# Performance work log

Hardware: AMD Instinct MI355X
Metric: run time of the kernel (lower is better)

The kernel has to match this reference:

```python
import jax, jax.numpy as jnp
import numpy as np

K = 4            # number of candidate kernels in Dynamic_conv2d
TEMP = 34.0      # softmax temperature (default in Dynamic_conv2d)
C = 64           # channel


def _dyn_conv(x, w, fc1_w, fc2_w, fc2_b, pad, dil):
    """Dynamic_conv2d forward.
    x: [B,Cin,H,W]; w: [K,Cout,Cin,k,k]; fc1_w: [hid,Cin]; fc2_w: [K,hid]; fc2_b: [K].
    """
    pooled = x.mean(axis=(2, 3))                                   # [B,Cin] adaptive avg pool
    h = jax.nn.relu(jnp.einsum('bc,hc->bh', pooled, fc1_w))        # [B,hid]
    logits = jnp.einsum('bh,kh->bk', h, fc2_w) + fc2_b             # [B,K]
    att = jax.nn.softmax(logits / TEMP, axis=-1)                   # [B,K]
    agg_w = jnp.einsum('bk,koihw->boihw', att, w)                  # per-sample kernel [B,Cout,Cin,k,k]

    def conv_one(xi, wi):
        return jax.lax.conv_general_dilated(
            xi[None], wi, window_strides=(1, 1),
            padding=[(pad, pad), (pad, pad)], rhs_dilation=(dil, dil),
            dimension_numbers=('NCHW', 'OIHW', 'NCHW'))[0]

    return jax.vmap(conv_one)(x, agg_w)                            # [B,Cout,H,W]


def _leaky(v):
    return jnp.where(v >= 0, v, 0.1 * v)


def _mk_params(key, cin, cout):
    hid = int(cin * 0.25) + 1
    k1, k2, k3, k4 = jax.random.split(key, 4)
    scale = np.sqrt(2.0 / (cin * 9)).astype(np.float32)
    w = jax.random.normal(k1, (K, cout, cin, 3, 3), jnp.float32) * scale
    fc1 = jax.random.normal(k2, (hid, cin), jnp.float32) * np.sqrt(2.0 / cin).astype(np.float32)
    fc2w = jax.random.normal(k3, (K, hid), jnp.float32) * np.sqrt(2.0 / hid).astype(np.float32)
    fc2b = jnp.zeros((K,), jnp.float32)
    return w, fc1, fc2w, fc2b


def setup_inputs() -> dict:
    key = jax.random.key(0)
    ks = jax.random.split(key, 5)
    x = jax.random.normal(ks[0], (16, C, 128, 128), jnp.float32)
    out = {'x': x}
    for i, (kk, cin) in enumerate(zip(ks[1:4], [C, C, C]), start=1):
        w, fc1, fc2w, fc2b = _mk_params(kk, cin, C)
        out[f'w{i}'], out[f'fc1_{i}'], out[f'fc2w_{i}'], out[f'fc2b_{i}'] = w, fc1, fc2w, fc2b
    w, fc1, fc2w, fc2b = _mk_params(ks[4], 3 * C, C)
    out['wt'], out['fc1_t'], out['fc2w_t'], out['fc2b_t'] = w, fc1, fc2w, fc2b
    return out


def reference(x, w1, fc1_1, fc2w_1, fc2b_1, w2, fc1_2, fc2w_2, fc2b_2,
              w3, fc1_3, fc2w_3, fc2b_3, wt, fc1_t, fc2w_t, fc2b_t):
    b1 = _leaky(_dyn_conv(x, w1, fc1_1, fc2w_1, fc2b_1, pad=1, dil=1))
    b2 = _leaky(_dyn_conv(x, w2, fc1_2, fc2w_2, fc2b_2, pad=2, dil=2))
    b3 = _leaky(_dyn_conv(x, w3, fc1_3, fc2w_3, fc2b_3, pad=4, dil=4))
    cat = jnp.concatenate([b1, b2, b3], axis=1)                    # [B,3C,H,W]
    return x + _dyn_conv(cat, wt, fc1_t, fc2w_t, fc2b_t, pad=1, dil=1)
```

## Files before the change

### kernel.cpp

```cpp
#include <hip/hip_runtime.h>
#include <hip/hip_bf16.h>

typedef __hip_bfloat16 bf16;
typedef __attribute__((ext_vector_type(4))) float f32x4;
typedef __attribute__((ext_vector_type(8))) short bf16x8;
typedef __attribute__((ext_vector_type(4))) short s16x4;

#define BB 16
#define HH 128
#define WW 128
#define HWSZ (HH*WW)
#define XH 136
#define XW 136
#define XPAD 4
#define CHH 130
#define CWD 130
#define CPAD 1
#define CATC 192

__device__ __forceinline__ void zero_border_body(bf16* __restrict__ base, int HP, int WP,
                                                 int PAD, int Cdim, int slots)
{
    int cg8 = Cdim >> 3;
    int per_b = slots * cg8;
    int idx = blockIdx.x * 256 + threadIdx.x;
    if (idx >= BB * per_b) return;
    int b = idx / per_b;
    int rem = idx - b * per_b;
    int slot = rem / cg8;
    int cg = rem - slot * cg8;
    int top = PAD * WP;
    int h, w;
    if (slot < top)            { h = slot / WP;            w = slot % WP; }
    else if (slot < 2 * top)   { int s = slot - top;       h = HP - PAD + s / WP; w = s % WP; }
    else {
        int s = slot - 2 * top;
        int row = s / (2 * PAD), t = s - row * (2 * PAD);
        h = PAD + row;
        w = (t < PAD) ? t : (WP - 2 * PAD + t);
    }
    bf16x8 z = {0,0,0,0,0,0,0,0};
    *(bf16x8*)(base + (((size_t)b * HP + h) * WP + w) * Cdim + cg * 8) = z;
}

__global__ void init_borders(bf16* __restrict__ xT, bf16* __restrict__ catT,
                             float* __restrict__ pooledx, float* __restrict__ pooledc)
{
    if (blockIdx.y == 0) {
        if (blockIdx.x == 0) {
            for (int i = threadIdx.x; i < BB * 64;   i += 256) pooledx[i] = 0.f;
            for (int i = threadIdx.x; i < BB * CATC; i += 256) pooledc[i] = 0.f;
        }
        zero_border_body(xT,   XH,  XW,  XPAD, 64,   2112);
    } else {
        zero_border_body(catT, CHH, CWD, CPAD, CATC, 516);
    }
}

__global__ __launch_bounds__(256)
void transpose_pad_pool_x(const float* __restrict__ x, bf16* __restrict__ xT,
                          float* __restrict__ pooledx)
{
    __shared__ float tile[128 * 65];
    const int h = blockIdx.x, b = blockIdx.y;
    const int t = threadIdx.x;
    const int w  = t & 127;
    const int chalf = t >> 7;

    const float* xb = x + (((size_t)b * 64) * HH + h) * WW + w;
    #pragma unroll
    for (int it = 0; it < 32; ++it) {
        int c = it * 2 + chalf;
        tile[w * 65 + c] = xb[(size_t)c * HWSZ];
    }
    __syncthreads();

    bf16* dst = xT + (((size_t)b * XH + (h + XPAD)) * XW + XPAD) * 64;
    #pragma unroll
    for (int it = 0; it < 4; ++it) {
        int v  = t + it * 256;
        int ww = v >> 3;
        int c0 = (v & 7) * 8;
        const float* src = tile + ww * 65 + c0;
        bf16x8 pk;
        #pragma unroll
        for (int j = 0; j < 8; ++j)
            pk[j] = __builtin_bit_cast(short, __float2bfloat16(src[j]));
        *(bf16x8*)(dst + (size_t)ww * 64 + c0) = pk;
    }

    if (t < 64) {
        float s = 0.f;
        #pragma unroll 4
        for (int ww = 0; ww < 128; ++ww) s += tile[ww * 65 + t];
        atomicAdd(pooledx + b * 64 + t, s);
    }
}

__device__ __forceinline__ void attn_body(int b, const float* pooled, int Cin,
                                          const float* fc1, int hid,
                                          const float* fc2w, const float* fc2b,
                                          float* att, float* sp, float* sh, float* slg)
{
    for (int c = threadIdx.x; c < Cin; c += 64) sp[c] = pooled[b * Cin + c];
    __syncthreads();
    int j = threadIdx.x;
    if (j < hid) {
        float s = 0.f;
        const float4* f4 = (const float4*)(fc1 + (size_t)j * Cin);
        for (int c4 = 0; c4 < Cin / 4; ++c4) {
            float4 v = f4[c4];
            s += v.x * sp[c4*4+0] + v.y * sp[c4*4+1] + v.z * sp[c4*4+2] + v.w * sp[c4*4+3];
        }
        sh[j] = s > 0.f ? s * (1.0f / 16384.0f) : 0.f;
    }
    __syncthreads();
    int k = threadIdx.x;
    if (k < 4) {
        float s = fc2b[k];
        for (int jj = 0; jj < hid; ++jj) s += fc2w[k * hid + jj] * sh[jj];
        slg[k] = s * (1.0f / 34.0f);
    }
    __syncthreads();
    if (threadIdx.x == 0) {
        float m = fmaxf(fmaxf(slg[0], slg[1]), fmaxf(slg[2], slg[3]));
        float e0 = expf(slg[0]-m), e1 = expf(slg[1]-m), e2 = expf(slg[2]-m), e3 = expf(slg[3]-m);
        float inv = 1.0f / (e0+e1+e2+e3);
        att[b*4+0] = e0*inv; att[b*4+1] = e1*inv; att[b*4+2] = e2*inv; att[b*4+3] = e3*inv;
    }
}

__global__ void attention3(const float* __restrict__ pooled,
                           const float* f1a, const float* f2a, const float* ba, float* aa,
                           const float* f1b, const float* f2b, const float* bb, float* ab,
                           const float* f1c, const float* f2c, const float* bc, float* ac)
{
    __shared__ float sp[192], sh[64], slg[4];
    int br = blockIdx.y;
    const float* fc1  = br == 0 ? f1a : br == 1 ? f1b : f1c;
    const float* fc2w = br == 0 ? f2a : br == 1 ? f2b : f2c;
    const float* fc2b = br == 0 ? ba  : br == 1 ? bb  : bc;
    float* att        = br == 0 ? aa  : br == 1 ? ab  : ac;
    attn_body(blockIdx.x, pooled, 64, fc1, 17, fc2w, fc2b, att, sp, sh, slg);
}

__global__ void attention_one(const float* __restrict__ pooled, int Cin,
                              const float* __restrict__ fc1, int hid,
                              const float* __restrict__ fc2w,
                              const float* __restrict__ fc2b, float* __restrict__ att)
{
    __shared__ float sp[192], sh[64], slg[4];
    attn_body(blockIdx.x, pooled, Cin, fc1, hid, fc2w, fc2b, att, sp, sh, slg);
}

template<int CIN, bool PERM>
__device__ __forceinline__ void aggw_body(const float* __restrict__ w,
                                          const float* __restrict__ att,
                                          bf16* __restrict__ out, float* wl)
{
    constexpr int C9 = CIN * 9;
    constexpr int NS = (CIN / 32) * 9;
    const int co = blockIdx.x, b = blockIdx.y;
    const int src = PERM ? ((co & 15) * 4 + (co >> 4)) : co;
    for (int i = threadIdx.x; i < 4 * C9; i += 256) {
        int k = i / C9, rem = i - k * C9;
        wl[i] = w[((size_t)k * 64 + src) * C9 + rem];
    }
    __syncthreads();
    float a0 = att[b*4+0], a1 = att[b*4+1], a2 = att[b*4+2], a3 = att[b*4+3];
    const int m = co >> 4, l15 = co & 15;
    char* ob = (char*)out + (size_t)b * NS * 4096;
    for (int t = threadIdx.x; t < NS * 32; t += 256) {
        int s = t >> 5, rem = t & 31;
        int gg = rem >> 3, j = rem & 7;
        int chunk = s / 9, tap = s - chunk * 9;
        int ci = chunk * 32 + gg * 8 + j;
        float v = a0 * wl[ci*9 + tap] + a1 * wl[C9 + ci*9 + tap]
                + a2 * wl[2*C9 + ci*9 + tap] + a3 * wl[3*C9 + ci*9 + tap];
        *(bf16*)(ob + ((size_t)((s*4 + m) * 64 + (gg*16 + l15))) * 16 + j * 2) = __float2bfloat16(v);
    }
}

__global__ void aggw_frag3(const float* __restrict__ w1, const float* __restrict__ att1, bf16* o1,
                           const float* __restrict__ w2, const float* __restrict__ att2, bf16* o2,
                           const float* __restrict__ w3, const float* __restrict__ att3, bf16* o3)
{
    __shared__ float wl[4 * 64 * 9];
    int z = blockIdx.z;
    if (z == 0)      aggw_body<64, true>(w1, att1, o1, wl);
    else if (z == 1) aggw_body<64, true>(w2, att2, o2, wl);
    else             aggw_body<64, true>(w3, att3, o3, wl);
}

__global__ void aggw_frag_t(const float* __restrict__ w, const float* __restrict__ att,
                            bf16* __restrict__ out)
{
    __shared__ float wl[4 * 192 * 9];
    aggw_body<192, false>(w, att, out, wl);
}

template<int DIL, int CIN>
__device__ __forceinline__ void conv_core(
    int b, int hb, int wt,
    const bf16* __restrict__ inT, int HPd, int WPd, int PAD,
    const bf16* __restrict__ aggwF,
    bf16* __restrict__ catT, int catbase, float* __restrict__ poolc,
    char* lds, float* sco)
{
    constexpr int NCHUNK = CIN / 32;
    constexpr int SLOTS  = 64 + 2 * DIL;
    constexpr int ROWB   = SLOTS * 64;
    constexpr int XBYTES = 10 * ROWB;
    constexpr int XSEG   = (XBYTES + 1023) / 1024;
    constexpr int ABYTES = 36864;
    constexpr int MAXT   = (XSEG + 7) / 8;

    const int r  = hb % DIL;
    const int q  = hb / DIL;
    const int tid  = threadIdx.x;
    const int wv   = tid >> 6;
    const int lane = tid & 63;
    const int n16  = lane & 15;
    const int g    = lane >> 4;

    const char* inB = (const char*)inT;
    const char* awB = (const char*)aggwF + (size_t)b * (NCHUNK * ABYTES);

    if (tid < 64) sco[tid] = 0.f;

    int baddr[12];
    #pragma unroll
    for (int nt = 0; nt < 4; ++nt)
        #pragma unroll
        for (int kw = 0; kw < 3; ++kw)
            baddr[nt*3+kw] = wv * ROWB + g * (SLOTS * 16)
                             + (nt * 16 + n16 + kw * DIL) * 16;

    int xoff[MAXT];
    #pragma unroll
    for (int t = 0; t < MAXT; ++t) {
        int i = wv + 8 * t;
        xoff[t] = 0;
        if (i < XSEG) {
            int o = i * 1024 + lane * 16;
            if (o < XBYTES) {
                int row  = o / ROWB;
                int rem  = o - row * ROWB;
                int g2   = rem / (SLOTS * 16);
                int slot = (rem - g2 * (SLOTS * 16)) >> 4;
                int h_in = (q * 8 + row - 1) * DIL + r;
                xoff[t] = ((b * HPd + PAD + h_in) * WPd + (PAD + wt * 64 - DIL + slot)) * (CIN * 2)
                          + g2 * 16;
            }
        }
    }

    auto stage = [&](int c) {
        #pragma unroll
        for (int t = 0; t < MAXT; ++t) {
            int i = wv + 8 * t;
            if (i >= XSEG) break;
            __builtin_amdgcn_global_load_lds(
                (const __attribute__((address_space(1))) void*)(inB + (size_t)(xoff[t] + c * 64)),
                (__attribute__((address_space(3))) void*)(lds + i * 1024), 16, 0, 0);
        }
    };

    f32x4 acc[4][4];
    #pragma unroll
    for (int nt = 0; nt < 4; ++nt)
        #pragma unroll
        for (int m = 0; m < 4; ++m) { f32x4 z = {0.f,0.f,0.f,0.f}; acc[nt][m] = z; }

    for (int c = 0; c < NCHUNK; ++c) {
        stage(c);
        __syncthreads();
        const char* awC = awB + (size_t)c * ABYTES + (size_t)lane * 16;
        #pragma unroll 3
        for (int tap = 0; tap < 9; ++tap) {
            const int kh = tap / 3, kw = tap - kh * 3;
            bf16x8 a[4];
            #pragma unroll
            for (int m = 0; m < 4; ++m)
                a[m] = *(const bf16x8*)(awC + (size_t)((tap * 4 + m) * 1024));
            #pragma unroll
            for (int nt = 0; nt < 4; ++nt) {
                const bf16x8 bfr = *(const bf16x8*)(lds + baddr[nt * 3 + kw] + kh * ROWB);
                #pragma unroll
                for (int m = 0; m < 4; ++m)
                    acc[nt][m] = __builtin_amdgcn_mfma_f32_16x16x32_bf16(a[m], bfr, acc[nt][m], 0, 0, 0);
            }
        }
        __syncthreads();
    }

    const int h_out = (q * 8 + wv) * DIL + r;
    float csum[4][4];
    #pragma unroll
    for (int m = 0; m < 4; ++m)
        #pragma unroll
        for (int qq = 0; qq < 4; ++qq) csum[m][qq] = 0.f;
    #pragma unroll
    for (int nt = 0; nt < 4; ++nt) {
        int w_out = wt * 64 + nt * 16 + n16;
        char* dst = (char*)(catT + (((size_t)b * CHH + (CPAD + h_out)) * CWD + (CPAD + w_out)) * CATC
                            + catbase) + g * 32;
        float lv[4][4];
        #pragma unroll
        for (int m = 0; m < 4; ++m)
            #pragma unroll
            for (int qq = 0; qq < 4; ++qq) {
                float v = acc[nt][m][qq];
                v = v >= 0.f ? v : 0.1f * v;
                lv[m][qq] = v;
                csum[m][qq] += v;
            }
        bf16x8 lo, hi;
        #pragma unroll
        for (int j = 0; j < 8; ++j) {
            lo[j] = __builtin_bit_cast(short, __float2bfloat16(lv[j & 3][j >> 2]));
            hi[j] = __builtin_bit_cast(short, __float2bfloat16(lv[j & 3][2 + (j >> 2)]));
        }
        *(bf16x8*)(dst)      = lo;
        *(bf16x8*)(dst + 16) = hi;
    }
    #pragma unroll
    for (int m = 0; m < 4; ++m)
        #pragma unroll
        for (int qq = 0; qq < 4; ++qq) {
            float v = csum[m][qq];
            v += __shfl_xor(v, 1, 64);
            v += __shfl_xor(v, 2, 64);
            v += __shfl_xor(v, 4, 64);
            v += __shfl_xor(v, 8, 64);
            if (n16 == 0) atomicAdd(&sco[g * 16 + qq * 4 + m], v);
        }
    __syncthreads();
    if (tid < 64) atomicAdd(poolc + b * CATC + catbase + tid, sco[tid]);
}

__global__ __launch_bounds__(512, 4)
void conv_branch3(const bf16* __restrict__ xT,
                  const bf16* __restrict__ aggF1, const bf16* __restrict__ aggF2,
                  const bf16* __restrict__ aggF3,
                  bf16* __restrict__ catT, float* __restrict__ poolc)
{
    constexpr int SCOO = 46080;
    __shared__ __align__(1024) char lds[SCOO + 256];
    float* sco = (float*)(lds + SCOO);

    const int bid  = blockIdx.x;
    const int xcd  = bid & 7;
    const int j    = bid >> 3;
    const int b    = 2 * xcd + (j >= 96 ? 1 : 0);
    const int u    = j % 96;
    const int band = u / 24;
    const int v    = u % 24;
    const int br   = v % 3;
    const int t2   = v / 3;
    const int wt   = t2 & 1;
    const int hb   = band * 4 + (t2 >> 1);

    if (br == 0)
        conv_core<1, 64>(b, hb, wt, xT, XH, XW, XPAD, aggF1, catT, 0,   poolc, lds, sco);
    else if (br == 1)
        conv_core<2, 64>(b, hb, wt, xT, XH, XW, XPAD, aggF2, catT, 64,  poolc, lds, sco);
    else
        conv_core<4, 64>(b, hb, wt, xT, XH, XW, XPAD, aggF3, catT, 128, poolc, lds, sco);
}

#define FF_ROWB 4224
#define FF_XBY  42240
#define FF_XSEG 42

__global__ __launch_bounds__(256, 2)
void conv_final(const bf16* __restrict__ catT, const bf16* __restrict__ aggFt,
                const float* __restrict__ x, float* __restrict__ out)
{
    __shared__ __align__(1024) char lds[FF_XSEG * 1024];

    const int bid = blockIdx.x;
    const int xcd = bid & 7;
    const int j   = bid >> 3;
    const int b   = 2 * xcd + (j >= 32 ? 1 : 0);
    const int u   = j & 31;
    const int wt  = u & 1;
    const int hb  = u >> 1;

    const int tid  = threadIdx.x;
    const int wv   = tid >> 6;
    const int lane = tid & 63;
    const int n16  = lane & 15;
    const int g    = lane >> 4;

    const char* inB = (const char*)catT;
    const char* awB = (const char*)aggFt + (size_t)b * (6 * 36864);

    int baddr[12];
    #pragma unroll
    for (int nt = 0; nt < 4; ++nt)
        #pragma unroll
        for (int kw = 0; kw < 3; ++kw)
            baddr[nt*3+kw] = (2 * wv) * FF_ROWB + g * (66 * 16) + (nt * 16 + n16 + kw) * 16;

    int xoff[11];
    #pragma unroll
    for (int t = 0; t < 11; ++t) {
        int i = wv + 4 * t;
        xoff[t] = 0;
        if (i < FF_XSEG) {
            int o = i * 1024 + lane * 16;
            if (o < FF_XBY) {
                int row  = o / FF_ROWB;
                int rem  = o - row * FF_ROWB;
                int g2   = rem / (66 * 16);
                int slot = (rem - g2 * (66 * 16)) >> 4;
                int h_in = hb * 8 + row - 1;
                xoff[t] = ((b * CHH + CPAD + h_in) * CWD + (CPAD + wt * 64 - 1 + slot)) * (CATC * 2)
                          + g2 * 16;
            }
        }
    }

    auto stage = [&](int c) {
        #pragma unroll
        for (int t = 0; t < 11; ++t) {
            int i = wv + 4 * t;
            if (i >= FF_XSEG) break;
            __builtin_amdgcn_global_load_lds(
                (const __attribute__((address_space(1))) void*)(inB + (size_t)(xoff[t] + c * 64)),
                (__attribute__((address_space(3))) void*)(lds + i * 1024), 16, 0, 0);
        }
    };

    f32x4 acc[2][4][4];
    #pragma unroll
    for (int orr = 0; orr < 2; ++orr)
        #pragma unroll
        for (int nt = 0; nt < 4; ++nt)
            #pragma unroll
            for (int m = 0; m < 4; ++m) { f32x4 z = {0.f,0.f,0.f,0.f}; acc[orr][nt][m] = z; }

    for (int c = 0; c < 6; ++c) {
        stage(c);
        __syncthreads();
        const char* awC = awB + (size_t)c * 36864 + (size_t)lane * 16;
        #pragma unroll
        for (int kw = 0; kw < 3; ++kw) {
            bf16x8 a[3][4];
            #pragma unroll
            for (int kh = 0; kh < 3; ++kh)
                #pragma unroll
                for (int m = 0; m < 4; ++m)
                    a[kh][m] = *(const bf16x8*)(awC + (size_t)(((kh * 3 + kw) * 4 + m) * 1024));
            #pragma unroll
            for (int nt = 0; nt < 4; ++nt) {
                bf16x8 bfr[4];
                #pragma unroll
                for (int rr = 0; rr < 4; ++rr)
                    bfr[rr] = *(const bf16x8*)(lds + baddr[nt * 3 + kw] + rr * FF_ROWB);
                #pragma unroll
                for (int kh = 0; kh < 3; ++kh)
                    #pragma unroll
                    for (int orr = 0; orr < 2; ++orr)
                        #pragma unroll
                        for (int m = 0; m < 4; ++m)
                            acc[orr][nt][m] = __builtin_amdgcn_mfma_f32_16x16x32_bf16(
                                a[kh][m], bfr[orr + kh], acc[orr][nt][m], 0, 0, 0);
            }
        }
        __syncthreads();
    }

    #pragma unroll
    for (int orr = 0; orr < 2; ++orr) {
        const int h_out = hb * 8 + 2 * wv + orr;
        #pragma unroll
        for (int nt = 0; nt < 4; ++nt) {
            int w_out = wt * 64 + nt * 16 + n16;
            #pragma unroll
            for (int m = 0; m < 4; ++m) {
                int co = m * 16 + g * 4;
                size_t base = (((size_t)b * 64 + co) * HH + h_out) * WW + w_out;
                #pragma unroll
                for (int qq = 0; qq < 4; ++qq) {
                    size_t idx = base + (size_t)qq * HWSZ;
                    out[idx] = x[idx] + acc[orr][nt][m][qq];
                }
            }
        }
    }
}

extern "C" void kernel_launch(void* const* d_in, const int* in_sizes, int n_in,
                              void* d_out, int out_size, void* d_ws, size_t ws_size,
                              hipStream_t stream) {
    const float* x      = (const float*)d_in[0];
    const float* w1     = (const float*)d_in[1];
    const float* fc1_1  = (const float*)d_in[2];
    const float* fc2w_1 = (const float*)d_in[3];
    const float* fc2b_1 = (const float*)d_in[4];
    const float* w2     = (const float*)d_in[5];
    const float* fc1_2  = (const float*)d_in[6];
    const float* fc2w_2 = (const float*)d_in[7];
    const float* fc2b_2 = (const float*)d_in[8];
    const float* w3     = (const float*)d_in[9];
    const float* fc1_3  = (const float*)d_in[10];
    const float* fc2w_3 = (const float*)d_in[11];
    const float* fc2b_3 = (const float*)d_in[12];
    const float* wt     = (const float*)d_in[13];
    const float* fc1_t  = (const float*)d_in[14];
    const float* fc2w_t = (const float*)d_in[15];
    const float* fc2b_t = (const float*)d_in[16];
    float* out = (float*)d_out;
    (void)in_sizes; (void)n_in; (void)out_size; (void)ws_size;

    char* ws = (char*)d_ws;
    auto alloc = [&](size_t bytes) { char* p = ws; ws += (bytes + 255) & ~(size_t)255; return p; };

    bf16*  aggF1   = (bf16*)alloc((size_t)BB * 18 * 4096);
    bf16*  aggF2   = (bf16*)alloc((size_t)BB * 18 * 4096);
    bf16*  aggF3   = (bf16*)alloc((size_t)BB * 18 * 4096);
    bf16*  aggFt   = (bf16*)alloc((size_t)BB * 54 * 4096);
    float* pooledx = (float*)alloc(BB * 64 * 4);
    float* pooledc = (float*)alloc(BB * 192 * 4);
    float* att1    = (float*)alloc(BB * 4 * 4);
    float* att2    = (float*)alloc(BB * 4 * 4);
    float* att3    = (float*)alloc(BB * 4 * 4);
    float* attt    = (float*)alloc(BB * 4 * 4);
    alloc(65536);
    const size_t XT_BYTES  = (size_t)BB * XH * XW * 64 * 2;
    bf16* xT   = (bf16*)alloc(XT_BYTES);
    alloc(65536);
    const size_t CAT_BYTES = (size_t)BB * CHH * CWD * CATC * 2;
    bf16* catT = (bf16*)alloc(CAT_BYTES);
    alloc(65536);

    init_borders<<<dim3(1056, 2), 256, 0, stream>>>(xT, catT, pooledx, pooledc);

    transpose_pad_pool_x<<<dim3(128, 16), 256, 0, stream>>>(x, xT, pooledx);

    attention3<<<dim3(16, 3), 64, 0, stream>>>(pooledx,
        fc1_1, fc2w_1, fc2b_1, att1,
        fc1_2, fc2w_2, fc2b_2, att2,
        fc1_3, fc2w_3, fc2b_3, att3);

    aggw_frag3<<<dim3(64, 16, 3), 256, 0, stream>>>(w1, att1, aggF1,
                                                    w2, att2, aggF2,
                                                    w3, att3, aggF3);

    conv_branch3<<<1536, 512, 0, stream>>>(xT, aggF1, aggF2, aggF3, catT, pooledc);

    attention_one<<<16, 64, 0, stream>>>(pooledc, CATC, fc1_t, 49, fc2w_t, fc2b_t, attt);
    aggw_frag_t<<<dim3(64, 16), 256, 0, stream>>>(wt, attt, aggFt);

    conv_final<<<512, 256, 0, stream>>>(catT, aggFt, x, out);
}
```

Measured before the change: 219.3 us.

## Compute two output rows per wave in branch conv to reuse weight fragments

The branch convolution kernel now uses 256 threads (4 waves), and each wave computes two output rows instead of one. Each weight A-fragment is loaded once per kw and reused across both rows. Four LDS input rows are loaded per nt and reused across the kh taps. This cuts the global/L2 weight loads and LDS reads per MFMA roughly in half. In exchange, accumulator register use doubles (128 floats), which may lower occupancy (launch bounds go from 512,4 to 256,2) and leave fewer waves to hide latency.

```diff
diff --git a/kernel.cpp b/kernel.cpp
--- a/kernel.cpp
+++ b/kernel.cpp
@@ -200,7 +200,7 @@
 }
 
 template<int DIL, int CIN>
-__device__ __forceinline__ void conv_core(
+__device__ __forceinline__ void conv_core2(
     int b, int hb, int wt,
     const bf16* __restrict__ inT, int HPd, int WPd, int PAD,
     const bf16* __restrict__ aggwF,
@@ -213,7 +213,7 @@
     constexpr int XBYTES = 10 * ROWB;
     constexpr int XSEG   = (XBYTES + 1023) / 1024;
     constexpr int ABYTES = 36864;
-    constexpr int MAXT   = (XSEG + 7) / 8;
+    constexpr int MAXT   = (XSEG + 3) / 4;
 
     const int r  = hb % DIL;
     const int q  = hb / DIL;
@@ -233,13 +233,13 @@
     for (int nt = 0; nt < 4; ++nt)
         #pragma unroll
         for (int kw = 0; kw < 3; ++kw)
-            baddr[nt*3+kw] = wv * ROWB + g * (SLOTS * 16)
+            baddr[nt*3+kw] = (2 * wv) * ROWB + g * (SLOTS * 16)
                              + (nt * 16 + n16 + kw * DIL) * 16;
 
     int xoff[MAXT];
     #pragma unroll
     for (int t = 0; t < MAXT; ++t) {
-        int i = wv + 8 * t;
+        int i = wv + 4 * t;
         xoff[t] = 0;
         if (i < XSEG) {
             int o = i * 1024 + lane * 16;
@@ -258,7 +258,7 @@
     auto stage = [&](int c) {
         #pragma unroll
         for (int t = 0; t < MAXT; ++t) {
-            int i = wv + 8 * t;
+            int i = wv + 4 * t;
             if (i >= XSEG) break;
             __builtin_amdgcn_global_load_lds(
                 (const __attribute__((address_space(1))) void*)(inB + (size_t)(xoff[t] + c * 64)),
@@ -266,63 +266,77 @@
         }
     };
 
-    f32x4 acc[4][4];
-    #pragma unroll
-    for (int nt = 0; nt < 4; ++nt)
-        #pragma unroll
-        for (int m = 0; m < 4; ++m) { f32x4 z = {0.f,0.f,0.f,0.f}; acc[nt][m] = z; }
+    f32x4 acc[2][4][4];
+    #pragma unroll
+    for (int orr = 0; orr < 2; ++orr)
+        #pragma unroll
+        for (int nt = 0; nt < 4; ++nt)
+            #pragma unroll
+            for (int m = 0; m < 4; ++m) { f32x4 z = {0.f,0.f,0.f,0.f}; acc[orr][nt][m] = z; }
 
     for (int c = 0; c < NCHUNK; ++c) {
         stage(c);
         __syncthreads();
         const char* awC = awB + (size_t)c * ABYTES + (size_t)lane * 16;
-        #pragma unroll 3
-        for (int tap = 0; tap < 9; ++tap) {
-            const int kh = tap / 3, kw = tap - kh * 3;
-            bf16x8 a[4];
+        #pragma unroll
+        for (int kw = 0; kw < 3; ++kw) {
+            bf16x8 a[3][4];
+            #pragma unroll
+            for (int kh = 0; kh < 3; ++kh)
+                #pragma unroll
+                for (int m = 0; m < 4; ++m)
+                    a[kh][m] = *(const bf16x8*)(awC + (size_t)(((kh * 3 + kw) * 4 + m) * 1024));
+            #pragma unroll
+            for (int nt = 0; nt < 4; ++nt) {
+                bf16x8 bfr[4];
+                #pragma unroll
+                for (int rr = 0; rr < 4; ++rr)
+                    bfr[rr] = *(const bf16x8*)(lds + baddr[nt * 3 + kw] + rr * ROWB);
+                #pragma unroll
+                for (int kh = 0; kh < 3; ++kh)
+                    #pragma unroll
+                    for (int orr = 0; orr < 2; ++orr)
+                        #pragma unroll
+                        for (int m = 0; m < 4; ++m)
+                            acc[orr][nt][m] = __builtin_amdgcn_mfma_f32_16x16x32_bf16(
+                                a[kh][m], bfr[orr + kh], acc[orr][nt][m], 0, 0, 0);
+            }
+        }
+        __syncthreads();
+    }
+
+    float csum[4][4];
+    #pragma unroll
+    for (int m = 0; m < 4; ++m)
+        #pragma unroll
+        for (int qq = 0; qq < 4; ++qq) csum[m][qq] = 0.f;
+    #pragma unroll
+    for (int orr = 0; orr < 2; ++orr) {
+        const int h_out = (q * 8 + 2 * wv + orr) * DIL + r;
+        #pragma unroll
+        for (int nt = 0; nt < 4; ++nt) {
+            int w_out = wt * 64 + nt * 16 + n16;
+            char* dst = (char*)(catT + (((size_t)b * CHH + (CPAD + h_out)) * CWD + (CPAD + w_out)) * CATC
+                                + catbase) + g * 32;
+            float lv[4][4];
             #pragma unroll
             for (int m = 0; m < 4; ++m)
-                a[m] = *(const bf16x8*)(awC + (size_t)((tap * 4 + m) * 1024));
-            #pragma unroll
-            for (int nt = 0; nt < 4; ++nt) {
-                const bf16x8 bfr = *(const bf16x8*)(lds + baddr[nt * 3 + kw] + kh * ROWB);
-                #pragma unroll
-                for (int m = 0; m < 4; ++m)
-                    acc[nt][m] = __builtin_amdgcn_mfma_f32_16x16x32_bf16(a[m], bfr, acc[nt][m], 0, 0, 0);
+                #pragma unroll
+                for (int qq = 0; qq < 4; ++qq) {
+                    float v = acc[orr][nt][m][qq];
+                    v = v >= 0.f ? v : 0.1f * v;
+                    lv[m][qq] = v;
+                    csum[m][qq] += v;
+                }
+            bf16x8 lo, hi;
+            #pragma unroll
+            for (int j = 0; j < 8; ++j) {
+                lo[j] = __builtin_bit_cast(short, __float2bfloat16(lv[j & 3][j >> 2]));
+                hi[j] = __builtin_bit_cast(short, __float2bfloat16(lv[j & 3][2 + (j >> 2)]));
             }
-        }
-        __syncthreads();
-    }
-
-    const int h_out = (q * 8 + wv) * DIL + r;
-    float csum[4][4];
-    #pragma unroll
-    for (int m = 0; m < 4; ++m)
-        #pragma unroll
-        for (int qq = 0; qq < 4; ++qq) csum[m][qq] = 0.f;
-    #pragma unroll
-    for (int nt = 0; nt < 4; ++nt) {
-        int w_out = wt * 64 + nt * 16 + n16;
-        char* dst = (char*)(catT + (((size_t)b * CHH + (CPAD + h_out)) * CWD + (CPAD + w_out)) * CATC
-                            + catbase) + g * 32;
-        float lv[4][4];
-        #pragma unroll
-        for (int m = 0; m < 4; ++m)
-            #pragma unroll
-            for (int qq = 0; qq < 4; ++qq) {
-                float v = acc[nt][m][qq];
-                v = v >= 0.f ? v : 0.1f * v;
-                lv[m][qq] = v;
-                csum[m][qq] += v;
-            }
-        bf16x8 lo, hi;
-        #pragma unroll
-        for (int j = 0; j < 8; ++j) {
-            lo[j] = __builtin_bit_cast(short, __float2bfloat16(lv[j & 3][j >> 2]));
-            hi[j] = __builtin_bit_cast(short, __float2bfloat16(lv[j & 3][2 + (j >> 2)]));
-        }
-        *(bf16x8*)(dst)      = lo;
-        *(bf16x8*)(dst + 16) = hi;
+            *(bf16x8*)(dst)      = lo;
+            *(bf16x8*)(dst + 16) = hi;
+        }
     }
     #pragma unroll
     for (int m = 0; m < 4; ++m)
@@ -339,7 +353,7 @@
     if (tid < 64) atomicAdd(poolc + b * CATC + catbase + tid, sco[tid]);
 }
 
-__global__ __launch_bounds__(512, 4)
+__global__ __launch_bounds__(256, 2)
 void conv_branch3(const bf16* __restrict__ xT,
                   const bf16* __restrict__ aggF1, const bf16* __restrict__ aggF2,
                   const bf16* __restrict__ aggF3,
@@ -362,11 +376,11 @@
     const int hb   = band * 4 + (t2 >> 1);
 
     if (br == 0)
-        conv_core<1, 64>(b, hb, wt, xT, XH, XW, XPAD, aggF1, catT, 0,   poolc, lds, sco);
+        conv_core2<1, 64>(b, hb, wt, xT, XH, XW, XPAD, aggF1, catT, 0,   poolc, lds, sco);
     else if (br == 1)
-        conv_core<2, 64>(b, hb, wt, xT, XH, XW, XPAD, aggF2, catT, 64,  poolc, lds, sco);
+        conv_core2<2, 64>(b, hb, wt, xT, XH, XW, XPAD, aggF2, catT, 64,  poolc, lds, sco);
     else
-        conv_core<4, 64>(b, hb, wt, xT, XH, XW, XPAD, aggF3, catT, 128, poolc, lds, sco);
+        conv_core2<4, 64>(b, hb, wt, xT, XH, XW, XPAD, aggF3, catT, 128, poolc, lds, sco);
 }
 
 #define FF_ROWB 4224
@@ -549,7 +563,7 @@
                                                     w2, att2, aggF2,
                                                     w3, att3, aggF3);
 
-    conv_branch3<<<1536, 512, 0, stream>>>(xT, aggF1, aggF2, aggF3, catT, pooledc);
+    conv_branch3<<<1536, 256, 0, stream>>>(xT, aggF1, aggF2, aggF3, catT, pooledc);
 
     attention_one<<<16, 64, 0, stream>>>(pooledc, CATC, fc1_t, 49, fc2w_t, fc2b_t, attt);
     aggw_frag_t<<<dim3(64, 16), 256, 0, stream>>>(wt, attt, aggFt);
```

Result: faster. 210.1 us (-4.2%).
